# Optimization experiments

Measured on AMD Instinct MI355X. Metric: run time of the kernel, lower is better.

The kernel has to match this reference:

```python
import jax, jax.numpy as jnp
import numpy as np
import math

B, T, S, C, W = 32, 512, 128, 30, 10  # batch, seq, spans, candidates, max span width
D_CTX, D_ENT, H, V = 768, 300, 100, 200000
EPS = 1e-5
NEG = -1e30


def layer_norm(x, g, b):
    mu = jnp.mean(x, axis=-1, keepdims=True)
    var = jnp.mean((x - mu) ** 2, axis=-1, keepdims=True)
    return (x - mu) / jnp.sqrt(var + EPS) * g + b


def setup_inputs() -> dict:
    key = jax.random.key(0)
    ks = jax.random.split(key, 12)
    contextual_embeddings = jax.random.normal(ks[0], (B, T, D_CTX), jnp.float32)
    mask = jnp.ones((B, T), jnp.int32)
    starts = jax.random.randint(ks[1], (B, S), 0, T - W)
    widths = jax.random.randint(ks[2], (B, S), 0, W)
    ends = starts + widths  # inclusive end, AllenNLP convention
    # pad last 8 spans per example with -1 to exercise span masking
    pad = jnp.arange(S)[None, :] >= S - 8
    starts = jnp.where(pad, -1, starts)
    ends = jnp.where(pad, -1, ends)
    candidate_spans = jnp.stack([starts, ends], axis=-1)
    candidate_entities = jax.random.randint(ks[3], (B, S, C), 1, V)
    pri = jax.random.uniform(ks[4], (B, S, C), jnp.float32)
    candidate_entity_priors = pri / pri.sum(-1, keepdims=True)
    candidate_segment_ids = jnp.zeros((B, S, C), jnp.int32)
    # parameters
    entity_table = jax.random.normal(ks[5], (V, D_ENT), jnp.float32) * 0.02
    proj_W = jax.random.normal(ks[6], (D_ENT, D_CTX), jnp.float32) * 0.02
    proj_b = jnp.zeros((D_ENT,), jnp.float32)
    kg_g = jnp.ones((D_ENT,), jnp.float32)
    kg_b = jnp.zeros((D_ENT,), jnp.float32)
    ln_g = jnp.ones((D_ENT,), jnp.float32)
    ln_b = jnp.zeros((D_ENT,), jnp.float32)
    attn_W = jax.random.normal(ks[7], (1, D_ENT), jnp.float32) * 0.02
    attn_b = jnp.zeros((1,), jnp.float32)
    W1 = jax.random.normal(ks[8], (H, 2), jnp.float32) * 0.02
    b1 = jnp.zeros((H,), jnp.float32)
    W2 = jax.random.normal(ks[9], (1, H), jnp.float32) * 0.02
    b2 = jnp.zeros((1,), jnp.float32)
    return dict(contextual_embeddings=contextual_embeddings, mask=mask,
                candidate_spans=candidate_spans, candidate_entities=candidate_entities,
                candidate_entity_priors=candidate_entity_priors,
                candidate_segment_ids=candidate_segment_ids,
                entity_table=entity_table, proj_W=proj_W, proj_b=proj_b,
                kg_g=kg_g, kg_b=kg_b, ln_g=ln_g, ln_b=ln_b,
                attn_W=attn_W, attn_b=attn_b, W1=W1, b1=b1, W2=W2, b2=b2)


def reference(contextual_embeddings, mask, candidate_spans, candidate_entities,
              candidate_entity_priors, candidate_segment_ids, entity_table,
              proj_W, proj_b, kg_g, kg_b, ln_g, ln_b, attn_W, attn_b,
              W1, b1, W2, b2):
    # --- entity embedding lookup + KG layer norm ---
    ent_emb = layer_norm(entity_table[candidate_entities], kg_g, kg_b)  # (B,S,C,D)

    # --- bert -> kg projection ---
    proj = contextual_embeddings @ proj_W.T + proj_b  # (B,T,D_ENT)

    span_mask = candidate_spans[:, :, 0] > -1  # (B,S)

    # --- SelfAttentiveSpanExtractor ---
    att_logits = (proj @ attn_W.T + attn_b)[..., 0]  # (B,T)
    starts = candidate_spans[..., 0]
    ends = candidate_spans[..., 1]
    widths = ends - starts
    offs = jnp.arange(W)  # max span width
    idx = starts[..., None] + offs  # (B,S,W)
    valid = (offs <= widths[..., None]) & (idx >= 0) & (idx < T)
    idx_c = jnp.where(valid, idx, 0)
    idx_flat = idx_c.reshape(B, S * W)
    span_emb = jnp.take_along_axis(proj, idx_flat[..., None], axis=1).reshape(B, S, W, D_ENT)
    span_log = jnp.take_along_axis(att_logits, idx_flat, axis=1).reshape(B, S, W)
    attn = jax.nn.softmax(jnp.where(valid, span_log, NEG), axis=-1)  # (B,S,W)
    span_rep = jnp.einsum('bsw,bswd->bsd', attn, span_emb)
    span_rep = span_rep * span_mask[..., None].astype(span_rep.dtype)
    span_rep = layer_norm(span_rep, ln_g, ln_b)  # (B,S,D)

    # --- DotAttentionWithPrior ---
    scores = jnp.einsum('bsd,bscd->bsc', span_rep, ent_emb) / math.sqrt(D_ENT)
    feat = jnp.stack([scores, candidate_entity_priors], axis=-1)  # (B,S,C,2)
    h = jax.nn.relu(feat @ W1.T + b1)
    link = (h @ W2.T + b2)[..., 0]  # (B,S,C)
    entity_mask = candidate_entities > 0
    linking_scores = jnp.where(entity_mask, link, -10000.0)
    normed = jax.nn.softmax(linking_scores, axis=-1)
    weighted = jnp.einsum('bsc,bscd->bsd', normed, ent_emb)
    return linking_scores, weighted
```

## Files before the change

kernel.cpp:

```cpp
#include <hip/hip_runtime.h>
#include <hip/hip_bf16.h>
#include <math.h>

#define BB 32
#define TT 512
#define SS 128
#define CC 30
#define WW 10
#define DCTX 768
#define DENT 300
#define HH 100
#define EPSF 1e-5f
#define NEGF -1e30f

typedef __attribute__((ext_vector_type(8))) short bf16x8;
typedef __attribute__((ext_vector_type(4))) float f32x4;

__device__ __forceinline__ float wave_sum(float v) {
    #pragma unroll
    for (int off = 32; off > 0; off >>= 1) v += __shfl_xor(v, off);
    return v;
}

__device__ __forceinline__ ushort f2bf(float f) {
    __hip_bfloat16 h = __float2bfloat16(f);
    return *reinterpret_cast<ushort*>(&h);
}

__device__ __forceinline__ float dot4(float4 a, float4 b) {
    return a.x*b.x + a.y*b.y + a.z*b.z + a.w*b.w;
}
__device__ __forceinline__ float hadd8(float4 a, float4 b) {
    return a.x+a.y+a.z+a.w + b.x+b.y+b.z+b.w;
}
__device__ __forceinline__ ushort4 cvt4(float4 v) {
    ushort4 h; h.x = f2bf(v.x); h.y = f2bf(v.y); h.z = f2bf(v.z); h.w = f2bf(v.w);
    return h;
}

#define GBM 64
#define GBK 32
#define LDA 40
#define LDB 40
#define NK  (DCTX / GBK)

__global__ __launch_bounds__(512) void gemm_proj_mfma(
    const float* __restrict__ A,
    const float* __restrict__ Wt,
    const float* __restrict__ bias,
    float* __restrict__ out)
{
    __shared__ ushort Al[2][GBM * LDA];
    __shared__ ushort Bl[2][320 * LDB];
    const int tid = threadIdx.x;
    const int lane = tid & 63;
    const int wv = tid >> 6;
    const int wm = wv >> 2;
    const int wn = wv & 3;
    const int m0 = blockIdx.x * GBM;
    const int ar = tid >> 3;
    const int ak = (tid & 7) * 4;
    const float4 z4 = make_float4(0.f, 0.f, 0.f, 0.f);

    int bn[5], bk[5];
    #pragma unroll
    for (int i = 0; i < 5; ++i) { int f = tid + i * 512; bn[i] = f >> 3; bk[i] = (f & 7) * 4; }

    const float* aP = A + (size_t)(m0 + ar) * DCTX + ak;

    f32x4 acc[2][5];
    #pragma unroll
    for (int i = 0; i < 2; ++i)
        #pragma unroll
        for (int j = 0; j < 5; ++j)
            acc[i][j] = (f32x4){0.f, 0.f, 0.f, 0.f};

    const int lr = lane & 15;
    const int kq = (lane >> 4) * 8;

    float4 avA, bvA[5], avB, bvB[5];

#define LOADSET(av_, bv_, K0) do {                                             \
        av_ = *(const float4*)(aP + (K0));                                     \
        _Pragma("unroll")                                                      \
        for (int i_ = 0; i_ < 5; ++i_)                                         \
            bv_[i_] = (bn[i_] < DENT)                                          \
                ? *(const float4*)(Wt + (size_t)bn[i_] * DCTX + (K0) + bk[i_]) \
                : z4;                                                          \
    } while (0)

#define STORESET(BUF, av_, bv_) do {                                           \
        *(ushort4*)&Al[BUF][ar * LDA + ak] = cvt4(av_);                        \
        _Pragma("unroll")                                                      \
        for (int i_ = 0; i_ < 5; ++i_)                                         \
            *(ushort4*)&Bl[BUF][bn[i_] * LDB + bk[i_]] = cvt4(bv_[i_]);        \
    } while (0)

#define COMPUTE(BUF) do {                                                      \
        bf16x8 af_[2], bf_[5];                                                 \
        _Pragma("unroll")                                                      \
        for (int i_ = 0; i_ < 2; ++i_)                                         \
            af_[i_] = *(const bf16x8*)&Al[BUF][(wm*32 + i_*16 + lr)*LDA + kq]; \
        _Pragma("unroll")                                                      \
        for (int j_ = 0; j_ < 5; ++j_)                                         \
            bf_[j_] = *(const bf16x8*)&Bl[BUF][(wn*80 + j_*16 + lr)*LDB + kq]; \
        _Pragma("unroll")                                                      \
        for (int i_ = 0; i_ < 2; ++i_)                                         \
            _Pragma("unroll")                                                  \
            for (int j_ = 0; j_ < 5; ++j_)                                     \
                acc[i_][j_] = __builtin_amdgcn_mfma_f32_16x16x32_bf16(         \
                    af_[i_], bf_[j_], acc[i_][j_], 0, 0, 0);                   \
    } while (0)

    LOADSET(avA, bvA, 0);
    LOADSET(avB, bvB, GBK);
    STORESET(0, avA, bvA);
    __syncthreads();

    #pragma unroll 1
    for (int kk = 0; kk < NK; kk += 2) {
        if (kk + 2 < NK) LOADSET(avA, bvA, (kk + 2) * GBK);
        COMPUTE(0);
        STORESET(1, avB, bvB);
        __syncthreads();
        if (kk + 3 < NK) LOADSET(avB, bvB, (kk + 3) * GBK);
        COMPUTE(1);
        if (kk + 2 < NK) STORESET(0, avA, bvA);
        __syncthreads();
    }

    const int lq = lane >> 4;
    #pragma unroll
    for (int j = 0; j < 5; ++j) {
        int col = wn * 80 + j * 16 + lr;
        if (col < DENT) {
            float bv = bias[col];
            #pragma unroll
            for (int i = 0; i < 2; ++i)
                #pragma unroll
                for (int r = 0; r < 4; ++r) {
                    int row = m0 + wm * 32 + i * 16 + lq * 4 + r;
                    out[(size_t)row * DENT + col] = acc[i][j][r] + bv;
                }
        }
    }
}

__global__ __launch_bounds__(256) void span_kernel(
    const float* __restrict__ proj,
    const int*   __restrict__ spans,
    const float* __restrict__ attn_W,
    const float* __restrict__ attn_b,
    const float* __restrict__ ln_g,
    const float* __restrict__ ln_b,
    const float* __restrict__ kg_g,
    const float* __restrict__ kg_b,
    float* __restrict__ srg_out,
    float* __restrict__ sgsb)
{
    const int bs = blockIdx.x * 4 + (threadIdx.x >> 6);
    const int b = bs >> 7;
    const int lane = threadIdx.x & 63;
    const int start = spans[bs * 2 + 0];
    const int end   = spans[bs * 2 + 1];
    const int width = end - start;
    const bool lo = lane < 11;
    const float4 z = make_float4(0.f, 0.f, 0.f, 0.f);

    const float4* attW4 = (const float4*)attn_W;
    float4 w0 = attW4[lane];
    float4 w1 = lo ? attW4[64 + lane] : z;

    float4 a0[WW], a1[WW];
    float slog[WW];
    bool vld[WW];
    #pragma unroll
    for (int w = 0; w < WW; ++w) {
        int idx = start + w;
        vld[w] = (w <= width) && (idx >= 0) && (idx < TT);
        const float4* pr = (const float4*)(proj + (size_t)(b * TT + (vld[w] ? idx : 0)) * DENT);
        a0[w] = pr[lane];
        a1[w] = lo ? pr[64 + lane] : z;
        slog[w] = dot4(a0[w], w0) + dot4(a1[w], w1);
    }
    const float ab = attn_b[0];
    #pragma unroll
    for (int w = 0; w < WW; ++w) {
        float r = wave_sum(slog[w]);
        slog[w] = vld[w] ? r + ab : NEGF;
    }
    float m = slog[0];
    #pragma unroll
    for (int w = 1; w < WW; ++w) m = fmaxf(m, slog[w]);
    float den = 0.f;
    float aw[WW];
    #pragma unroll
    for (int w = 0; w < WW; ++w) { aw[w] = expf(slog[w] - m); den += aw[w]; }
    const float inv = 1.f / den;
    const float msk = (start > -1) ? inv : 0.f;

    float4 acc0 = z, acc1 = z;
    #pragma unroll
    for (int w = 0; w < WW; ++w) {
        float c = aw[w] * msk;
        acc0.x = fmaf(c, a0[w].x, acc0.x); acc0.y = fmaf(c, a0[w].y, acc0.y);
        acc0.z = fmaf(c, a0[w].z, acc0.z); acc0.w = fmaf(c, a0[w].w, acc0.w);
        acc1.x = fmaf(c, a1[w].x, acc1.x); acc1.y = fmaf(c, a1[w].y, acc1.y);
        acc1.z = fmaf(c, a1[w].z, acc1.z); acc1.w = fmaf(c, a1[w].w, acc1.w);
    }
    float s1 = hadd8(acc0, acc1);
    float s2 = dot4(acc0, acc0) + dot4(acc1, acc1);
    #pragma unroll
    for (int off = 32; off > 0; off >>= 1) {
        s1 += __shfl_xor(s1, off);
        s2 += __shfl_xor(s2, off);
    }
    const float mu = s1 * (1.f / DENT);
    const float rstd = rsqrtf(s2 * (1.f / DENT) - mu * mu + EPSF);

    const float4* lg4 = (const float4*)ln_g;  const float4* lb4 = (const float4*)ln_b;
    const float4* gg4 = (const float4*)kg_g;  const float4* gb4 = (const float4*)kg_b;
    float pg = 0.f, pb = 0.f;
    float4* so = (float4*)(srg_out + (size_t)bs * DENT);
    {
        float4 g = lg4[lane], bb_ = lb4[lane], gg = gg4[lane], gb = gb4[lane];
        float4 val;
        val.x = fmaf((acc0.x - mu) * rstd, g.x, bb_.x);
        val.y = fmaf((acc0.y - mu) * rstd, g.y, bb_.y);
        val.z = fmaf((acc0.z - mu) * rstd, g.z, bb_.z);
        val.w = fmaf((acc0.w - mu) * rstd, g.w, bb_.w);
        float4 vg = make_float4(val.x * gg.x, val.y * gg.y, val.z * gg.z, val.w * gg.w);
        so[lane] = vg;
        pg += vg.x + vg.y + vg.z + vg.w;
        pb += val.x * gb.x + val.y * gb.y + val.z * gb.z + val.w * gb.w;
    }
    if (lo) {
        float4 g = lg4[64 + lane], bb_ = lb4[64 + lane], gg = gg4[64 + lane], gb = gb4[64 + lane];
        float4 val;
        val.x = fmaf((acc1.x - mu) * rstd, g.x, bb_.x);
        val.y = fmaf((acc1.y - mu) * rstd, g.y, bb_.y);
        val.z = fmaf((acc1.z - mu) * rstd, g.z, bb_.z);
        val.w = fmaf((acc1.w - mu) * rstd, g.w, bb_.w);
        float4 vg = make_float4(val.x * gg.x, val.y * gg.y, val.z * gg.z, val.w * gg.w);
        so[64 + lane] = vg;
        pg += vg.x + vg.y + vg.z + vg.w;
        pb += val.x * gb.x + val.y * gb.y + val.z * gb.z + val.w * gb.w;
    }
    #pragma unroll
    for (int off = 32; off > 0; off >>= 1) {
        pg += __shfl_xor(pg, off);
        pb += __shfl_xor(pb, off);
    }
    if (lane == 0) { sgsb[bs * 2 + 0] = pg; sgsb[bs * 2 + 1] = pb; }
}

__global__ __launch_bounds__(512) void final_fused(
    const float* __restrict__ srg,
    const float* __restrict__ sgsb,
    const int*   __restrict__ cand,
    const float* __restrict__ priors,
    const float* __restrict__ table,
    const float* __restrict__ W1,
    const float* __restrict__ b1,
    const float* __restrict__ W2,
    const float* __restrict__ b2,
    const float* __restrict__ kg_g,
    const float* __restrict__ kg_b,
    float* __restrict__ out_link,
    float* __restrict__ out_w)
{
    __shared__ float rows[CC][DENT];
    __shared__ float smu[CC], srs[CC], ssc[CC], sexp[CC];
    const int bs = blockIdx.x;
    const int tid = threadIdx.x;
    const int lane = tid & 63;
    const int wv = tid >> 6;
    const bool lo = lane < 11;
    const float4 z = make_float4(0.f, 0.f, 0.f, 0.f);

    const int c0 = wv, c1 = wv + 8, c2 = wv + 16, c3 = wv + 24;
    const bool has3 = (c3 < CC);
    const int e0 = cand[bs * CC + c0];
    const int e1 = cand[bs * CC + c1];
    const int e2 = cand[bs * CC + c2];
    const int e3 = has3 ? cand[bs * CC + c3] : e2;

    const float4* r0 = (const float4*)(table + (size_t)e0 * DENT);
    const float4* r1 = (const float4*)(table + (size_t)e1 * DENT);
    const float4* r2 = (const float4*)(table + (size_t)e2 * DENT);
    const float4* r3 = (const float4*)(table + (size_t)e3 * DENT);
    float4 xa0 = r0[lane], xa1 = r1[lane], xa2 = r2[lane], xa3 = r3[lane];
    float4 xb0 = lo ? r0[64 + lane] : z;
    float4 xb1 = lo ? r1[64 + lane] : z;
    float4 xb2 = lo ? r2[64 + lane] : z;
    float4 xb3 = lo ? r3[64 + lane] : z;

    const float4* sg4 = (const float4*)(srg + (size_t)bs * DENT);
    float4 g0 = sg4[lane];
    float4 g1 = lo ? sg4[64 + lane] : z;
    const float SG = sgsb[bs * 2 + 0];
    const float SB = sgsb[bs * 2 + 1];

    const float W1a0 = W1[2 * lane], W1b0 = W1[2 * lane + 1];
    const float B10 = b1[lane], W20 = W2[lane];
    float W1a1 = 0.f, W1b1 = 0.f, B11 = 0.f, W21 = 0.f;
    if (lane < HH - 64) {
        int j = lane + 64;
        W1a1 = W1[2 * j]; W1b1 = W1[2 * j + 1]; B11 = b1[j]; W21 = W2[j];
    }
    const float b2v = b2[0];
    const float p0 = priors[bs * CC + c0];
    const float p1 = priors[bs * CC + c1];
    const float p2 = priors[bs * CC + c2];
    const float p3 = has3 ? priors[bs * CC + c3] : 0.f;

    *(float4*)&rows[c0][lane * 4] = xa0;
    *(float4*)&rows[c1][lane * 4] = xa1;
    *(float4*)&rows[c2][lane * 4] = xa2;
    if (has3) *(float4*)&rows[c3][lane * 4] = xa3;
    if (lo) {
        *(float4*)&rows[c0][256 + lane * 4] = xb0;
        *(float4*)&rows[c1][256 + lane * 4] = xb1;
        *(float4*)&rows[c2][256 + lane * 4] = xb2;
        if (has3) *(float4*)&rows[c3][256 + lane * 4] = xb3;
    }

    float s1_0 = hadd8(xa0, xb0), s1_1 = hadd8(xa1, xb1);
    float s1_2 = hadd8(xa2, xb2), s1_3 = hadd8(xa3, xb3);
    float s2_0 = dot4(xa0, xa0) + dot4(xb0, xb0), s2_1 = dot4(xa1, xa1) + dot4(xb1, xb1);
    float s2_2 = dot4(xa2, xa2) + dot4(xb2, xb2), s2_3 = dot4(xa3, xa3) + dot4(xb3, xb3);
    float s3_0 = dot4(g0, xa0) + dot4(g1, xb0), s3_1 = dot4(g0, xa1) + dot4(g1, xb1);
    float s3_2 = dot4(g0, xa2) + dot4(g1, xb2), s3_3 = dot4(g0, xa3) + dot4(g1, xb3);
    #pragma unroll
    for (int off = 32; off > 0; off >>= 1) {
        s1_0 += __shfl_xor(s1_0, off); s1_1 += __shfl_xor(s1_1, off);
        s1_2 += __shfl_xor(s1_2, off); s1_3 += __shfl_xor(s1_3, off);
        s2_0 += __shfl_xor(s2_0, off); s2_1 += __shfl_xor(s2_1, off);
        s2_2 += __shfl_xor(s2_2, off); s2_3 += __shfl_xor(s2_3, off);
        s3_0 += __shfl_xor(s3_0, off); s3_1 += __shfl_xor(s3_1, off);
        s3_2 += __shfl_xor(s3_2, off); s3_3 += __shfl_xor(s3_3, off);
    }
    const float isd = rsqrtf((float)DENT);

#define CAND_TAIL(K, CK, EK, PK)                                               \
    do {                                                                       \
        float mu_ = s1_##K * (1.f / DENT);                                     \
        float rstd_ = rsqrtf(s2_##K * (1.f / DENT) - mu_ * mu_ + EPSF);        \
        float score_ = (rstd_ * (s3_##K - mu_ * SG) + SB) * isd;               \
        float h_ = fmaxf(fmaf(W1a0, score_, fmaf(W1b0, PK, B10)), 0.f);        \
        float h2_ = fmaxf(fmaf(W1a1, score_, fmaf(W1b1, PK, B11)), 0.f);       \
        float lp_ = fmaf(W21, h2_, W20 * h_);                                  \
        lp_ = wave_sum(lp_) + b2v;                                             \
        float link_ = (EK > 0) ? lp_ : -10000.0f;                              \
        if (lane == 0) {                                                       \
            smu[CK] = mu_; srs[CK] = rstd_; ssc[CK] = link_;                   \
            out_link[bs * CC + CK] = link_;                                    \
        }                                                                      \
    } while (0)

    CAND_TAIL(0, c0, e0, p0);
    CAND_TAIL(1, c1, e1, p1);
    CAND_TAIL(2, c2, e2, p2);
    if (has3) CAND_TAIL(3, c3, e3, p3);
    __syncthreads();

    if (tid < CC) {
        float m = ssc[0];
        #pragma unroll
        for (int c = 1; c < CC; ++c) m = fmaxf(m, ssc[c]);
        sexp[tid] = expf(ssc[tid] - m);
    }
    __syncthreads();

    const int d = tid;
    if (d < DENT) {
        float den = 0.f;
        #pragma unroll
        for (int c = 0; c < CC; ++c) den += sexp[c];
        const float inv = 1.f / den;
        float acc = 0.f, S2 = 0.f, sn = 0.f;
        #pragma unroll
        for (int c = 0; c < CC; ++c) {
            float n = sexp[c] * inv;
            float coef = n * srs[c];
            acc = fmaf(coef, rows[c][d], acc);
            S2 = fmaf(coef, smu[c], S2);
            sn += n;
        }
        out_w[(size_t)bs * DENT + d] = kg_g[d] * (acc - S2) + kg_b[d] * sn;
    }
}

extern "C" void kernel_launch(void* const* d_in, const int* in_sizes, int n_in,
                              void* d_out, int out_size, void* d_ws, size_t ws_size,
                              hipStream_t stream) {
    const float* ctx    = (const float*)d_in[0];
    const int*   spans  = (const int*)d_in[2];
    const int*   cand   = (const int*)d_in[3];
    const float* priors = (const float*)d_in[4];
    const float* table  = (const float*)d_in[6];
    const float* projW  = (const float*)d_in[7];
    const float* projb  = (const float*)d_in[8];
    const float* kg_g   = (const float*)d_in[9];
    const float* kg_b   = (const float*)d_in[10];
    const float* ln_g   = (const float*)d_in[11];
    const float* ln_b   = (const float*)d_in[12];
    const float* attW   = (const float*)d_in[13];
    const float* attb   = (const float*)d_in[14];
    const float* W1     = (const float*)d_in[15];
    const float* b1     = (const float*)d_in[16];
    const float* W2     = (const float*)d_in[17];
    const float* b2     = (const float*)d_in[18];

    float* proj = (float*)d_ws;
    float* srg  = proj + (size_t)BB * TT * DENT;
    float* sgsb = srg + (size_t)BB * SS * DENT;

    float* out_link = (float*)d_out;
    float* out_w    = out_link + (size_t)BB * SS * CC;

    gemm_proj_mfma<<<dim3(BB * TT / GBM), 512, 0, stream>>>(ctx, projW, projb, proj);
    span_kernel<<<BB * SS / 4, 256, 0, stream>>>(proj, spans, attW, attb,
                                                 ln_g, ln_b, kg_g, kg_b, srg, sgsb);
    final_fused<<<BB * SS, 512, 0, stream>>>(srg, sgsb, cand, priors, table,
                                             W1, b1, W2, b2, kg_g, kg_b,
                                             out_link, out_w);
}
```

Measured before the change: 97.31 us.

## Pre-pack projection weights into MFMA fragment order and drop LDS staging

A new pre-pass kernel converts the projection weight to bf16 and stores it in the exact per-lane MFMA fragment order, reusing the srg workspace region before span_kernel writes it. The GEMM then loads A and B fragments directly from global memory into registers with one-step register prefetch, removing shared-memory staging and the barriers around it. Blocks shrink to 32 rows and 256 threads, so there are twice as many blocks. The cost is an extra launch, repeated weight reads from global or L2 memory by every block with no LDS reuse, and uncoalesced-looking A row loads.

```diff
diff --git a/kernel.cpp b/kernel.cpp
--- a/kernel.cpp
+++ b/kernel.cpp
@@ -16,6 +16,9 @@
 typedef __attribute__((ext_vector_type(8))) short bf16x8;
 typedef __attribute__((ext_vector_type(4))) float f32x4;
 
+#define NK  (DCTX / 32)
+#define NCT 20
+
 __device__ __forceinline__ float wave_sum(float v) {
     #pragma unroll
     for (int off = 32; off > 0; off >>= 1) v += __shfl_xor(v, off);
@@ -33,40 +36,51 @@
 __device__ __forceinline__ float hadd8(float4 a, float4 b) {
     return a.x+a.y+a.z+a.w + b.x+b.y+b.z+b.w;
 }
-__device__ __forceinline__ ushort4 cvt4(float4 v) {
-    ushort4 h; h.x = f2bf(v.x); h.y = f2bf(v.y); h.z = f2bf(v.z); h.w = f2bf(v.w);
-    return h;
-}
-
-#define GBM 64
-#define GBK 32
-#define LDA 40
-#define LDB 40
-#define NK  (DCTX / GBK)
-
-__global__ __launch_bounds__(512) void gemm_proj_mfma(
-    const float* __restrict__ A,
-    const float* __restrict__ Wt,
-    const float* __restrict__ bias,
+__device__ __forceinline__ bf16x8 cvt8(float4 u, float4 v) {
+    bf16x8 r;
+    r[0] = (short)f2bf(u.x); r[1] = (short)f2bf(u.y);
+    r[2] = (short)f2bf(u.z); r[3] = (short)f2bf(u.w);
+    r[4] = (short)f2bf(v.x); r[5] = (short)f2bf(v.y);
+    r[6] = (short)f2bf(v.z); r[7] = (short)f2bf(v.w);
+    return r;
+}
+
+__global__ __launch_bounds__(256) void wpre_kernel(
+    const float* __restrict__ Wt, ushort* __restrict__ wpre)
+{
+    const int g = blockIdx.x * 256 + threadIdx.x;
+    const int l = g & 63;
+    const int t = (g >> 6) % NK;
+    const int ct = g / (NK * 64);
+    const int col = ct * 16 + (l & 15);
+    const int k = t * 32 + (l >> 4) * 8;
+    ushort4 h0 = {0, 0, 0, 0}, h1 = {0, 0, 0, 0};
+    if (col < DENT) {
+        float4 v0 = *(const float4*)(Wt + (size_t)col * DCTX + k);
+        float4 v1 = *(const float4*)(Wt + (size_t)col * DCTX + k + 4);
+        h0.x = f2bf(v0.x); h0.y = f2bf(v0.y); h0.z = f2bf(v0.z); h0.w = f2bf(v0.w);
+        h1.x = f2bf(v1.x); h1.y = f2bf(v1.y); h1.z = f2bf(v1.z); h1.w = f2bf(v1.w);
+    }
+    *(ushort4*)(wpre + (size_t)g * 8)     = h0;
+    *(ushort4*)(wpre + (size_t)g * 8 + 4) = h1;
+}
+
+__global__ __launch_bounds__(256) void gemm_proj_mfma(
+    const float*  __restrict__ A,
+    const ushort* __restrict__ wpre,
+    const float*  __restrict__ bias,
     float* __restrict__ out)
 {
-    __shared__ ushort Al[2][GBM * LDA];
-    __shared__ ushort Bl[2][320 * LDB];
     const int tid = threadIdx.x;
     const int lane = tid & 63;
-    const int wv = tid >> 6;
-    const int wm = wv >> 2;
-    const int wn = wv & 3;
-    const int m0 = blockIdx.x * GBM;
-    const int ar = tid >> 3;
-    const int ak = (tid & 7) * 4;
-    const float4 z4 = make_float4(0.f, 0.f, 0.f, 0.f);
-
-    int bn[5], bk[5];
-    #pragma unroll
-    for (int i = 0; i < 5; ++i) { int f = tid + i * 512; bn[i] = f >> 3; bk[i] = (f & 7) * 4; }
-
-    const float* aP = A + (size_t)(m0 + ar) * DCTX + ak;
+    const int wn = tid >> 6;
+    const int m0 = blockIdx.x * 32;
+    const int lr = lane & 15;
+    const int kq = (lane >> 4) * 8;
+
+    const float* a0p = A + (size_t)(m0 + lr) * DCTX + kq;
+    const float* a1p = a0p + (size_t)16 * DCTX;
+    const ushort* bp = wpre + (size_t)wn * 5 * NK * 512 + (size_t)lane * 8;
 
     f32x4 acc[2][5];
     #pragma unroll
@@ -75,58 +89,39 @@
         for (int j = 0; j < 5; ++j)
             acc[i][j] = (f32x4){0.f, 0.f, 0.f, 0.f};
 
-    const int lr = lane & 15;
-    const int kq = (lane >> 4) * 8;
-
-    float4 avA, bvA[5], avB, bvB[5];
-
-#define LOADSET(av_, bv_, K0) do {                                             \
-        av_ = *(const float4*)(aP + (K0));                                     \
-        _Pragma("unroll")                                                      \
-        for (int i_ = 0; i_ < 5; ++i_)                                         \
-            bv_[i_] = (bn[i_] < DENT)                                          \
-                ? *(const float4*)(Wt + (size_t)bn[i_] * DCTX + (K0) + bk[i_]) \
-                : z4;                                                          \
-    } while (0)
-
-#define STORESET(BUF, av_, bv_) do {                                           \
-        *(ushort4*)&Al[BUF][ar * LDA + ak] = cvt4(av_);                        \
-        _Pragma("unroll")                                                      \
-        for (int i_ = 0; i_ < 5; ++i_)                                         \
-            *(ushort4*)&Bl[BUF][bn[i_] * LDB + bk[i_]] = cvt4(bv_[i_]);        \
-    } while (0)
-
-#define COMPUTE(BUF) do {                                                      \
-        bf16x8 af_[2], bf_[5];                                                 \
-        _Pragma("unroll")                                                      \
-        for (int i_ = 0; i_ < 2; ++i_)                                         \
-            af_[i_] = *(const bf16x8*)&Al[BUF][(wm*32 + i_*16 + lr)*LDA + kq]; \
-        _Pragma("unroll")                                                      \
-        for (int j_ = 0; j_ < 5; ++j_)                                         \
-            bf_[j_] = *(const bf16x8*)&Bl[BUF][(wn*80 + j_*16 + lr)*LDB + kq]; \
-        _Pragma("unroll")                                                      \
-        for (int i_ = 0; i_ < 2; ++i_)                                         \
-            _Pragma("unroll")                                                  \
-            for (int j_ = 0; j_ < 5; ++j_)                                     \
-                acc[i_][j_] = __builtin_amdgcn_mfma_f32_16x16x32_bf16(         \
-                    af_[i_], bf_[j_], acc[i_][j_], 0, 0, 0);                   \
-    } while (0)
-
-    LOADSET(avA, bvA, 0);
-    LOADSET(avB, bvB, GBK);
-    STORESET(0, avA, bvA);
-    __syncthreads();
+    float4 ca0, ca1, ca2, ca3;
+    bf16x8 cb[5];
+    ca0 = *(const float4*)(a0p);     ca1 = *(const float4*)(a0p + 4);
+    ca2 = *(const float4*)(a1p);     ca3 = *(const float4*)(a1p + 4);
+    #pragma unroll
+    for (int j = 0; j < 5; ++j)
+        cb[j] = *(const bf16x8*)(bp + (size_t)j * NK * 512);
 
     #pragma unroll 1
-    for (int kk = 0; kk < NK; kk += 2) {
-        if (kk + 2 < NK) LOADSET(avA, bvA, (kk + 2) * GBK);
-        COMPUTE(0);
-        STORESET(1, avB, bvB);
-        __syncthreads();
-        if (kk + 3 < NK) LOADSET(avB, bvB, (kk + 3) * GBK);
-        COMPUTE(1);
-        if (kk + 2 < NK) STORESET(0, avA, bvA);
-        __syncthreads();
+    for (int t = 0; t < NK; ++t) {
+        float4 na0, na1, na2, na3;
+        bf16x8 nb[5];
+        if (t + 1 < NK) {
+            const float* ap = a0p + (t + 1) * 32;
+            na0 = *(const float4*)(ap);
+            na1 = *(const float4*)(ap + 4);
+            na2 = *(const float4*)(ap + (size_t)16 * DCTX);
+            na3 = *(const float4*)(ap + (size_t)16 * DCTX + 4);
+            #pragma unroll
+            for (int j = 0; j < 5; ++j)
+                nb[j] = *(const bf16x8*)(bp + ((size_t)j * NK + t + 1) * 512);
+        }
+        bf16x8 af0 = cvt8(ca0, ca1);
+        bf16x8 af1 = cvt8(ca2, ca3);
+        #pragma unroll
+        for (int j = 0; j < 5; ++j)
+            acc[0][j] = __builtin_amdgcn_mfma_f32_16x16x32_bf16(af0, cb[j], acc[0][j], 0, 0, 0);
+        #pragma unroll
+        for (int j = 0; j < 5; ++j)
+            acc[1][j] = __builtin_amdgcn_mfma_f32_16x16x32_bf16(af1, cb[j], acc[1][j], 0, 0, 0);
+        ca0 = na0; ca1 = na1; ca2 = na2; ca3 = na3;
+        #pragma unroll
+        for (int j = 0; j < 5; ++j) cb[j] = nb[j];
     }
 
     const int lq = lane >> 4;
@@ -139,7 +134,7 @@
             for (int i = 0; i < 2; ++i)
                 #pragma unroll
                 for (int r = 0; r < 4; ++r) {
-                    int row = m0 + wm * 32 + i * 16 + lq * 4 + r;
+                    int row = m0 + i * 16 + lq * 4 + r;
                     out[(size_t)row * DENT + col] = acc[i][j][r] + bv;
                 }
         }
@@ -415,11 +410,13 @@
     float* proj = (float*)d_ws;
     float* srg  = proj + (size_t)BB * TT * DENT;
     float* sgsb = srg + (size_t)BB * SS * DENT;
+    ushort* wpre = (ushort*)srg;
 
     float* out_link = (float*)d_out;
     float* out_w    = out_link + (size_t)BB * SS * CC;
 
-    gemm_proj_mfma<<<dim3(BB * TT / GBM), 512, 0, stream>>>(ctx, projW, projb, proj);
+    wpre_kernel<<<NCT * NK * 64 / 256, 256, 0, stream>>>(projW, wpre);
+    gemm_proj_mfma<<<BB * TT / 32, 256, 0, stream>>>(ctx, wpre, projb, proj);
     span_kernel<<<BB * SS / 4, 256, 0, stream>>>(proj, spans, attW, attb,
                                                  ln_g, ln_b, kg_g, kg_b, srg, sgsb);
     final_fused<<<BB * SS, 512, 0, stream>>>(srg, sgsb, cand, priors, table,
```

Result: slower. 105.7 us (+8.6%).
